# Optimization experiments

Hardware: AMD Instinct MI355X
Metric: run time of the kernel (lower is better)

Reference implementation:

```python
import jax, jax.numpy as jnp
import numpy as np
import math

B, S, HID, NH = 4, 2048, 1024, 16
HD = HID // NH  # head dim = 64


def setup_inputs() -> dict:
    key = jax.random.key(0)
    ks = jax.random.split(key, 8)
    sc = 0.02
    return {
        "x": jax.random.normal(ks[0], (B, S, HID), dtype=jnp.float32),
        "att_mask": jnp.zeros((B, 1, 1, S), dtype=jnp.float32),
        "Wq": jax.random.normal(ks[1], (HID, HID), dtype=jnp.float32) * sc,
        "bq": jax.random.normal(ks[2], (HID,), dtype=jnp.float32) * sc,
        "Wk": jax.random.normal(ks[3], (HID, HID), dtype=jnp.float32) * sc,
        "bk": jax.random.normal(ks[4], (HID,), dtype=jnp.float32) * sc,
        "Wv": jax.random.normal(ks[5], (HID, HID), dtype=jnp.float32) * sc,
        "bv": jax.random.normal(ks[6], (HID,), dtype=jnp.float32) * sc,
    }


def reference(x, att_mask, Wq, bq, Wk, bk, Wv, bv):
    # quant_mode=False path: QuantLinear acts as a plain affine projection
    # (the running min/max stats only calibrate `scale`, which is unused in
    # the float path), and IntSoftmax reduces to a standard softmax.
    q = x @ Wq.T + bq  # [B,S,HID]
    k = x @ Wk.T + bk
    v = x @ Wv.T + bv
    # split heads: [B,S,HID] -> [B,NH,S,HD]
    q = q.reshape(B, S, NH, HD).transpose(0, 2, 1, 3)
    k = k.reshape(B, S, NH, HD).transpose(0, 2, 1, 3)
    v = v.reshape(B, S, NH, HD).transpose(0, 2, 1, 3)
    scores = jnp.einsum("bhqd,bhkd->bhqk", q, k) / math.sqrt(HD) + att_mask
    probs = jax.nn.softmax(scores, axis=-1)  # [B,NH,S,S]
    ctx = jnp.einsum("bhqk,bhkd->bhqd", probs, v)  # [B,NH,S,HD]
    return ctx.transpose(0, 2, 1, 3).reshape(B, S, HID)
```

## Files before the change

### kernel.cpp

```cpp
#include <hip/hip_runtime.h>
#include <hip/hip_bf16.h>
#include <cstdint>
#include <cstddef>

#define BB   4
#define SS   2048
#define HIDD 1024
#define NHH  16
#define HDD  64
#define MM   (BB*SS)
#define L2E  1.4426950408889634f
#define SH4  5.770780163555854f

typedef __bf16    bf16x8 __attribute__((ext_vector_type(8)));
typedef float     f32x4  __attribute__((ext_vector_type(4)));
typedef _Float16  half4  __attribute__((ext_vector_type(4)));
typedef _Float16  half8  __attribute__((ext_vector_type(8)));
typedef _Float16  half2v __attribute__((ext_vector_type(2)));
typedef unsigned  u32x4  __attribute__((ext_vector_type(4)));

__device__ __forceinline__ unsigned short f2b(float f) {
    unsigned u = __builtin_bit_cast(unsigned, f);
    return (unsigned short)((u + 0x7FFFu + ((u >> 16) & 1u)) >> 16);
}

__device__ __forceinline__ half2v pkrtz(float a, float b) {
    return __builtin_bit_cast(half2v, __builtin_amdgcn_cvt_pkrtz(a, b));
}

__device__ __forceinline__ unsigned pkrtz_u(float a, float b) {
    return __builtin_bit_cast(unsigned, __builtin_amdgcn_cvt_pkrtz(a, b));
}

__device__ __forceinline__ void gl_lds16(const void* g, void* l) {
    __builtin_amdgcn_global_load_lds(
        (const __attribute__((address_space(1))) void*)g,
        (__attribute__((address_space(3))) void*)l, 16, 0, 0);
}

#define NX4 (MM * HIDD / 4)
#define NW4 (HIDD * HIDD / 4)
__global__ __launch_bounds__(256) void cvt_all(
    const float* __restrict__ x,  const float* __restrict__ wq,
    const float* __restrict__ wk, const float* __restrict__ wv,
    unsigned short* __restrict__ xb, unsigned short* __restrict__ wb)
{
    int i = blockIdx.x * 256 + threadIdx.x;
    const float* src; unsigned short* dst; int off;
    if (i < NX4) { src = x; dst = xb; off = i; }
    else {
        int j = i - NX4;
        int w = j >> 18;
        off = j & (NW4 - 1);
        src = (w == 0) ? wq : (w == 1) ? wk : wv;
        dst = wb + (size_t)w * HIDD * HIDD;
    }
    float4 v = reinterpret_cast<const float4*>(src)[off];
    ushort4 o;
    o.x = f2b(v.x); o.y = f2b(v.y); o.z = f2b(v.z); o.w = f2b(v.w);
    reinterpret_cast<ushort4*>(dst)[off] = o;
}

__global__ __launch_bounds__(256, 3) void qkv_gemm(
    const unsigned short* __restrict__ xb,
    const unsigned short* __restrict__ wb,
    const float* __restrict__ bq, const float* __restrict__ bk, const float* __restrict__ bv,
    unsigned short* __restrict__ Qb, unsigned short* __restrict__ Kb,
    _Float16* __restrict__ Vtb)
{
    __shared__ unsigned short lA[128 * 64];
    __shared__ unsigned short lB[128 * 64];

    const int tid  = threadIdx.x;
    const int wave = tid >> 6, lane = tid & 63;
    const int lh   = lane & 15, quad = lane >> 4;
    const int l7   = lh & 7;
    const int m0   = blockIdx.x * 128;
    const int opn  = blockIdx.y;
    const int op   = opn >> 3;
    const int n0   = (opn & 7) * 128;
    const unsigned short* W = wb + (size_t)op * HIDD * HIDD;
    const float* bias = (op == 0) ? bq : (op == 1) ? bk : bv;

    f32x4 acc[4][4];
#pragma unroll
    for (int i = 0; i < 4; i++)
#pragma unroll
        for (int j = 0; j < 4; j++) acc[i][j] = f32x4{0.f, 0.f, 0.f, 0.f};

    const int wm = wave & 1, wn = wave >> 1;
    const unsigned short* srcA = (op == 2) ? lA : lB;
    const unsigned short* srcB = (op == 2) ? lB : lA;
    const int offA = (op == 2) ? wm : wn;
    const int offB = (op == 2) ? wn : wm;

    const int srow = tid >> 3;
    const int sg   = tid & 7;

    for (int k0 = 0; k0 < HIDD; k0 += 64) {
#pragma unroll
        for (int rr = 0; rr < 4; rr++) {
            const int row = srow + rr * 32;
            const int gcol = k0 + ((sg ^ (row & 7)) << 3);
            gl_lds16(&xb[(size_t)(m0 + row) * HIDD + gcol], &lA[row * 64 + sg * 8]);
            gl_lds16(&W [(size_t)(n0 + row) * HIDD + gcol], &lB[row * 64 + sg * 8]);
        }
        __syncthreads();

#pragma unroll
        for (int kk = 0; kk < 2; kk++) {
            bf16x8 aF[4], bF[4];
#pragma unroll
            for (int i = 0; i < 4; i++) {
                const int row = offA * 64 + i * 16 + lh;
                aF[i] = *reinterpret_cast<const bf16x8*>(
                    &srcA[row * 64 + (((kk * 4 + quad) ^ l7) << 3)]);
            }
#pragma unroll
            for (int j = 0; j < 4; j++) {
                const int row = offB * 64 + j * 16 + lh;
                bF[j] = *reinterpret_cast<const bf16x8*>(
                    &srcB[row * 64 + (((kk * 4 + quad) ^ l7) << 3)]);
            }
#pragma unroll
            for (int i = 0; i < 4; i++)
#pragma unroll
                for (int j = 0; j < 4; j++)
                    acc[i][j] = __builtin_amdgcn_mfma_f32_16x16x32_bf16(aF[i], bF[j], acc[i][j], 0, 0, 0);
        }
        __syncthreads();
    }

    if (op == 2) {
#pragma unroll
        for (int j = 0; j < 4; j++) {
            const int n = n0 + offB * 64 + j * 16 + lh;
            const float bvv = bias[n];
            const int h = n >> 6, d = n & 63;
#pragma unroll
            for (int i = 0; i < 4; i++) {
                const int mrow = m0 + offA * 64 + i * 16 + quad * 4;
                const int b_ = mrow >> 11, s_ = mrow & 2047;
                half2v h01 = pkrtz(acc[i][j][0] + bvv, acc[i][j][1] + bvv);
                half2v h23 = pkrtz(acc[i][j][2] + bvv, acc[i][j][3] + bvv);
                half4 hv; hv[0] = h01[0]; hv[1] = h01[1]; hv[2] = h23[0]; hv[3] = h23[1];
                size_t a = ((size_t)(b_ * NHH + h) * HDD + d) * SS + s_;
                *reinterpret_cast<half4*>(&Vtb[a]) = hv;
            }
        }
    } else {
        const float qs = (op == 0) ? (0.125f * L2E) : 1.0f;
        unsigned short* dst = (op == 0) ? Qb : Kb;
#pragma unroll
        for (int i = 0; i < 4; i++) {
            const int nb = n0 + offA * 64 + i * 16 + quad * 4;
            const float4 bb = *reinterpret_cast<const float4*>(&bias[nb]);
            const int h = nb >> 6, d = nb & 63;
#pragma unroll
            for (int j = 0; j < 4; j++) {
                const int m = m0 + offB * 64 + j * 16 + lh;
                const int b_ = m >> 11, s_ = m & 2047;
                ushort4 o;
                o.x = f2b((acc[i][j][0] + bb.x) * qs);
                o.y = f2b((acc[i][j][1] + bb.y) * qs);
                o.z = f2b((acc[i][j][2] + bb.z) * qs);
                o.w = f2b((acc[i][j][3] + bb.w) * qs);
                *reinterpret_cast<ushort4*>(
                    &dst[((size_t)(b_ * NHH + h) * SS + s_) * HDD + d]) = o;
            }
        }
    }
}

__global__ __launch_bounds__(256, 4) void attn_kernel(
    const unsigned short* __restrict__ Qb,
    const unsigned short* __restrict__ Kb,
    const _Float16* __restrict__ Vtb,
    const float* __restrict__ mask,
    float* __restrict__ out)
{
    __shared__ unsigned short lK[2][64 * 64];
    __shared__ _Float16      lV[2][64 * 64];
    __shared__ float         lmm[SS];

    const int tid  = threadIdx.x;
    const int wave = tid >> 6, lane = tid & 63;
    const int lh   = lane & 15, quad = lane >> 4;
    const int l7   = lh & 7;
    const int bh = blockIdx.x, qt = blockIdx.y;
    const int b = bh >> 4, h = bh & 15;
    const unsigned short* Qh = Qb  + (size_t)bh * SS * HDD;
    const unsigned short* Kh = Kb  + (size_t)bh * SS * HDD;
    const _Float16*       Vh = Vtb + (size_t)bh * HDD * SS;
    const float* mk = mask + (size_t)b * SS;
    const int q0 = qt * 128;

    bf16x8 qF[2][2];
#pragma unroll
    for (int i = 0; i < 2; i++)
#pragma unroll
        for (int kk = 0; kk < 2; kk++)
            qF[i][kk] = *reinterpret_cast<const bf16x8*>(
                &Qh[(size_t)(q0 + wave * 32 + i * 16 + lh) * HDD + kk * 32 + quad * 8]);

    f32x4 oacc[2][4];
#pragma unroll
    for (int i = 0; i < 2; i++)
#pragma unroll
        for (int dj = 0; dj < 4; dj++) oacc[i][dj] = f32x4{0.f, 0.f, 0.f, 0.f};
    f32x4 osum[2] = {f32x4{0.f, 0.f, 0.f, 0.f}, f32x4{0.f, 0.f, 0.f, 0.f}};

    const u32x4 one_u = {0x3C003C00u, 0x3C003C00u, 0x3C003C00u, 0x3C003C00u};
    const half8 vone  = __builtin_bit_cast(half8, one_u);

    const int srow = tid >> 3;
    const int sg   = tid & 7;

#define STAGE(KT, BUF) do {                                                     \
    const int kb_ = (KT) * 64;                                                  \
    _Pragma("unroll")                                                           \
    for (int rr = 0; rr < 2; rr++) {                                            \
        const int row = srow + rr * 32;                                         \
        const int swk = ((sg ^ ((row & 3) | ((row >> 1) & 4))) << 3);           \
        const int swv = ((sg ^ (row & 7)) << 3);                                \
        gl_lds16(&Kh[(size_t)(kb_ + row) * HDD + swk], &lK[BUF][row * 64 + sg * 8]); \
        gl_lds16(&Vh[(size_t)row * SS + kb_ + swv],    &lV[BUF][row * 64 + sg * 8]); \
    }                                                                           \
} while (0)

    STAGE(0, 0);

#pragma unroll
    for (int j = 0; j < 2; j++) {
        const int idx = tid * 8 + j * 4;
        float4 m = *reinterpret_cast<const float4*>(&mk[idx]);
        float4 r;
        r.x = __builtin_fmaf(m.x, L2E, -SH4);
        r.y = __builtin_fmaf(m.y, L2E, -SH4);
        r.z = __builtin_fmaf(m.z, L2E, -SH4);
        r.w = __builtin_fmaf(m.w, L2E, -SH4);
        *reinterpret_cast<float4*>(&lmm[idx]) = r;
    }
    __syncthreads();

    for (int kt = 0; kt < SS / 64; kt++) {
        if (kt < SS / 64 - 1) STAGE(kt + 1, (kt + 1) & 1);
        const int buf = kt & 1;
        const int kb = kt * 64;

        unsigned pw[2][2][4];
#pragma unroll
        for (int t = 0; t < 2; t++) {
#pragma unroll
            for (int a = 0; a < 2; a++) {
                const int key = t * 32 + ((lh & 12) << 1) + (a << 2) + (lh & 3);
                const int krow = key * 64;
                bf16x8 kf0 = *reinterpret_cast<const bf16x8*>(
                    &lK[buf][krow + ((quad ^ l7) << 3)]);
                bf16x8 kf1 = *reinterpret_cast<const bf16x8*>(
                    &lK[buf][krow + (((4 + quad) ^ l7) << 3)]);
                const f32x4 mm = *reinterpret_cast<const f32x4*>(
                    &lmm[kb + t * 32 + quad * 8 + a * 4]);
#pragma unroll
                for (int i = 0; i < 2; i++) {
                    f32x4 s = __builtin_amdgcn_mfma_f32_16x16x32_bf16(kf0, qF[i][0], mm, 0, 0, 0);
                    s = __builtin_amdgcn_mfma_f32_16x16x32_bf16(kf1, qF[i][1], s, 0, 0, 0);
                    pw[t][i][a * 2 + 0] = pkrtz_u(__builtin_amdgcn_exp2f(s[0]),
                                                  __builtin_amdgcn_exp2f(s[1]));
                    pw[t][i][a * 2 + 1] = pkrtz_u(__builtin_amdgcn_exp2f(s[2]),
                                                  __builtin_amdgcn_exp2f(s[3]));
                }
            }
        }

        __builtin_amdgcn_s_setprio(1);
#pragma unroll
        for (int t = 0; t < 2; t++) {
            half8 vf[4];
#pragma unroll
            for (int dj = 0; dj < 4; dj++)
                vf[dj] = *reinterpret_cast<const half8*>(
                    &lV[buf][(dj * 16 + lh) * 64 + (((t * 4 + quad) ^ l7) << 3)]);
#pragma unroll
            for (int i = 0; i < 2; i++) {
                const u32x4 pu = {pw[t][i][0], pw[t][i][1], pw[t][i][2], pw[t][i][3]};
                const half8 pF = __builtin_bit_cast(half8, pu);
                osum[i] = __builtin_amdgcn_mfma_f32_16x16x32_f16(vone, pF, osum[i], 0, 0, 0);
#pragma unroll
                for (int dj = 0; dj < 4; dj++)
                    oacc[i][dj] = __builtin_amdgcn_mfma_f32_16x16x32_f16(
                        vf[dj], pF, oacc[i][dj], 0, 0, 0);
            }
        }
        __builtin_amdgcn_s_setprio(0);
        if (kt < SS / 64 - 1) __syncthreads();
    }

#pragma unroll
    for (int i = 0; i < 2; i++) {
        const float rls = 1.0f / osum[i][0];
        const int q = q0 + wave * 32 + i * 16 + lh;
#pragma unroll
        for (int dj = 0; dj < 4; dj++) {
            float4 o4;
            o4.x = oacc[i][dj][0] * rls;
            o4.y = oacc[i][dj][1] * rls;
            o4.z = oacc[i][dj][2] * rls;
            o4.w = oacc[i][dj][3] * rls;
            *reinterpret_cast<float4*>(
                &out[((size_t)b * SS + q) * HIDD + h * HDD + dj * 16 + quad * 4]) = o4;
        }
    }
}

extern "C" void kernel_launch(void* const* d_in, const int* in_sizes, int n_in,
                              void* d_out, int out_size, void* d_ws, size_t ws_size,
                              hipStream_t stream) {
    const float* x    = (const float*)d_in[0];
    const float* mask = (const float*)d_in[1];
    const float* Wq   = (const float*)d_in[2];
    const float* bq   = (const float*)d_in[3];
    const float* Wk   = (const float*)d_in[4];
    const float* bk   = (const float*)d_in[5];
    const float* Wv   = (const float*)d_in[6];
    const float* bv   = (const float*)d_in[7];
    float* out = (float*)d_out;
    (void)in_sizes; (void)n_in; (void)out_size; (void)ws_size;

    unsigned short* ws  = (unsigned short*)d_ws;
    unsigned short* xb  = ws;
    unsigned short* wb  = xb + (size_t)MM * HIDD;
    unsigned short* Qb  = wb + (size_t)3 * HIDD * HIDD;
    unsigned short* Kb  = Qb + (size_t)MM * HIDD;
    _Float16*       Vtb = (_Float16*)(Kb + (size_t)MM * HIDD);

    cvt_all<<<(NX4 + 3 * NW4) / 256, 256, 0, stream>>>(x, Wq, Wk, Wv, xb, wb);

    qkv_gemm<<<dim3(MM / 128, 24), 256, 0, stream>>>(xb, wb, bq, bk, bv, Qb, Kb, Vtb);

    attn_kernel<<<dim3(BB * NHH, SS / 128), 256, 0, stream>>>(Qb, Kb, Vtb, mask, out);
}
```

Measured before the change: 236.2 us.

## Software-pipeline attention tile: defer second-half PV MFMA into next iteration

```diff
diff --git a/kernel.cpp b/kernel.cpp
--- a/kernel.cpp
+++ b/kernel.cpp
@@ -228,6 +228,61 @@
     }                                                                           \
 } while (0)
 
+#define A_HALF(T, PF) do {                                                     \
+    _Pragma("unroll")                                                          \
+    for (int a = 0; a < 2; a++) {                                              \
+        const int key = (T) * 32 + ((lh & 12) << 1) + (a << 2) + (lh & 3);     \
+        const int krow = key * 64;                                             \
+        bf16x8 kf0 = *reinterpret_cast<const bf16x8*>(                         \
+            &lK[buf][krow + ((quad ^ l7) << 3)]);                              \
+        bf16x8 kf1 = *reinterpret_cast<const bf16x8*>(                         \
+            &lK[buf][krow + (((4 + quad) ^ l7) << 3)]);                        \
+        const f32x4 mm = *reinterpret_cast<const f32x4*>(                      \
+            &lmm[kb + (T) * 32 + quad * 8 + a * 4]);                           \
+        _Pragma("unroll")                                                      \
+        for (int i = 0; i < 2; i++) {                                          \
+            f32x4 s = __builtin_amdgcn_mfma_f32_16x16x32_bf16(kf0, qF[i][0], mm, 0, 0, 0); \
+            s = __builtin_amdgcn_mfma_f32_16x16x32_bf16(kf1, qF[i][1], s, 0, 0, 0);        \
+            PF[i][a * 2 + 0] = pkrtz_u(__builtin_amdgcn_exp2f(s[0]),           \
+                                       __builtin_amdgcn_exp2f(s[1]));          \
+            PF[i][a * 2 + 1] = pkrtz_u(__builtin_amdgcn_exp2f(s[2]),           \
+                                       __builtin_amdgcn_exp2f(s[3]));          \
+        }                                                                      \
+    }                                                                          \
+} while (0)
+
+#define LOADV(T, VF) do {                                                      \
+    _Pragma("unroll")                                                          \
+    for (int dj = 0; dj < 4; dj++)                                             \
+        VF[dj] = *reinterpret_cast<const half8*>(                              \
+            &lV[buf][(dj * 16 + lh) * 64 + ((((T) * 4 + quad) ^ l7) << 3)]);   \
+} while (0)
+
+#define PV_HALF(PF, VF) do {                                                   \
+    __builtin_amdgcn_s_setprio(1);                                             \
+    _Pragma("unroll")                                                          \
+    for (int i = 0; i < 2; i++) {                                              \
+        const u32x4 pu = {PF[i][0], PF[i][1], PF[i][2], PF[i][3]};             \
+        const half8 pF = __builtin_bit_cast(half8, pu);                        \
+        osum[i] = __builtin_amdgcn_mfma_f32_16x16x32_f16(vone, pF, osum[i], 0, 0, 0); \
+        _Pragma("unroll")                                                      \
+        for (int dj = 0; dj < 4; dj++)                                         \
+            oacc[i][dj] = __builtin_amdgcn_mfma_f32_16x16x32_f16(              \
+                VF[dj], pF, oacc[i][dj], 0, 0, 0);                             \
+    }                                                                          \
+    __builtin_amdgcn_s_setprio(0);                                             \
+} while (0)
+
+    unsigned pfc[2][4];
+    half8    vfc[4];
+#pragma unroll
+    for (int i = 0; i < 2; i++)
+#pragma unroll
+        for (int w = 0; w < 4; w++) pfc[i][w] = 0u;
+#pragma unroll
+    for (int dj = 0; dj < 4; dj++)
+        vfc[dj] = __builtin_bit_cast(half8, u32x4{0u, 0u, 0u, 0u});
+
     STAGE(0, 0);
 
 #pragma unroll
@@ -248,53 +303,20 @@
         const int buf = kt & 1;
         const int kb = kt * 64;
 
-        unsigned pw[2][2][4];
-#pragma unroll
-        for (int t = 0; t < 2; t++) {
-#pragma unroll
-            for (int a = 0; a < 2; a++) {
-                const int key = t * 32 + ((lh & 12) << 1) + (a << 2) + (lh & 3);
-                const int krow = key * 64;
-                bf16x8 kf0 = *reinterpret_cast<const bf16x8*>(
-                    &lK[buf][krow + ((quad ^ l7) << 3)]);
-                bf16x8 kf1 = *reinterpret_cast<const bf16x8*>(
-                    &lK[buf][krow + (((4 + quad) ^ l7) << 3)]);
-                const f32x4 mm = *reinterpret_cast<const f32x4*>(
-                    &lmm[kb + t * 32 + quad * 8 + a * 4]);
-#pragma unroll
-                for (int i = 0; i < 2; i++) {
-                    f32x4 s = __builtin_amdgcn_mfma_f32_16x16x32_bf16(kf0, qF[i][0], mm, 0, 0, 0);
-                    s = __builtin_amdgcn_mfma_f32_16x16x32_bf16(kf1, qF[i][1], s, 0, 0, 0);
-                    pw[t][i][a * 2 + 0] = pkrtz_u(__builtin_amdgcn_exp2f(s[0]),
-                                                  __builtin_amdgcn_exp2f(s[1]));
-                    pw[t][i][a * 2 + 1] = pkrtz_u(__builtin_amdgcn_exp2f(s[2]),
-                                                  __builtin_amdgcn_exp2f(s[3]));
-                }
-            }
-        }
-
-        __builtin_amdgcn_s_setprio(1);
-#pragma unroll
-        for (int t = 0; t < 2; t++) {
-            half8 vf[4];
-#pragma unroll
-            for (int dj = 0; dj < 4; dj++)
-                vf[dj] = *reinterpret_cast<const half8*>(
-                    &lV[buf][(dj * 16 + lh) * 64 + (((t * 4 + quad) ^ l7) << 3)]);
-#pragma unroll
-            for (int i = 0; i < 2; i++) {
-                const u32x4 pu = {pw[t][i][0], pw[t][i][1], pw[t][i][2], pw[t][i][3]};
-                const half8 pF = __builtin_bit_cast(half8, pu);
-                osum[i] = __builtin_amdgcn_mfma_f32_16x16x32_f16(vone, pF, osum[i], 0, 0, 0);
-#pragma unroll
-                for (int dj = 0; dj < 4; dj++)
-                    oacc[i][dj] = __builtin_amdgcn_mfma_f32_16x16x32_f16(
-                        vf[dj], pF, oacc[i][dj], 0, 0, 0);
-            }
-        }
-        __builtin_amdgcn_s_setprio(0);
+        PV_HALF(pfc, vfc);
+
+        unsigned pf0[2][4];
+        A_HALF(0, pf0);
+        half8 vf0[4];
+        LOADV(0, vf0);
+        PV_HALF(pf0, vf0);
+
+        A_HALF(1, pfc);
+        LOADV(1, vfc);
+
         if (kt < SS / 64 - 1) __syncthreads();
     }
+    PV_HALF(pfc, vfc);
 
 #pragma unroll
     for (int i = 0; i < 2; i++) {
@@ -311,6 +333,10 @@
                 &out[((size_t)b * SS + q) * HIDD + h * HDD + dj * 16 + quad * 4]) = o4;
         }
     }
+#undef PV_HALF
+#undef LOADV
+#undef A_HALF
+#undef STAGE
 }
 
 extern "C" void kernel_launch(void* const* d_in, const int* in_sizes, int n_in,
```

New measurement: 235.3 us (median of 3 runs). About the same (-0.4%).

## Double per-wave query rows in attention and read mask directly from global

Applied to the files above, without the earlier changes.

```diff
diff --git a/kernel.cpp b/kernel.cpp
--- a/kernel.cpp
+++ b/kernel.cpp
@@ -172,7 +172,7 @@
     }
 }
 
-__global__ __launch_bounds__(256, 4) void attn_kernel(
+__global__ __launch_bounds__(256, 2) void attn_kernel(
     const unsigned short* __restrict__ Qb,
     const unsigned short* __restrict__ Kb,
     const _Float16* __restrict__ Vtb,
@@ -181,7 +181,6 @@
 {
     __shared__ unsigned short lK[2][64 * 64];
     __shared__ _Float16      lV[2][64 * 64];
-    __shared__ float         lmm[SS];
 
     const int tid  = threadIdx.x;
     const int wave = tid >> 6, lane = tid & 63;
@@ -193,22 +192,24 @@
     const unsigned short* Kh = Kb  + (size_t)bh * SS * HDD;
     const _Float16*       Vh = Vtb + (size_t)bh * HDD * SS;
     const float* mk = mask + (size_t)b * SS;
-    const int q0 = qt * 128;
-
-    bf16x8 qF[2][2];
-#pragma unroll
-    for (int i = 0; i < 2; i++)
+    const int q0 = qt * 256;
+
+    bf16x8 qF[4][2];
+#pragma unroll
+    for (int i = 0; i < 4; i++)
 #pragma unroll
         for (int kk = 0; kk < 2; kk++)
             qF[i][kk] = *reinterpret_cast<const bf16x8*>(
-                &Qh[(size_t)(q0 + wave * 32 + i * 16 + lh) * HDD + kk * 32 + quad * 8]);
-
-    f32x4 oacc[2][4];
-#pragma unroll
-    for (int i = 0; i < 2; i++)
+                &Qh[(size_t)(q0 + wave * 64 + i * 16 + lh) * HDD + kk * 32 + quad * 8]);
+
+    f32x4 oacc[4][4];
+#pragma unroll
+    for (int i = 0; i < 4; i++)
 #pragma unroll
         for (int dj = 0; dj < 4; dj++) oacc[i][dj] = f32x4{0.f, 0.f, 0.f, 0.f};
-    f32x4 osum[2] = {f32x4{0.f, 0.f, 0.f, 0.f}, f32x4{0.f, 0.f, 0.f, 0.f}};
+    f32x4 osum[4];
+#pragma unroll
+    for (int i = 0; i < 4; i++) osum[i] = f32x4{0.f, 0.f, 0.f, 0.f};
 
     const u32x4 one_u = {0x3C003C00u, 0x3C003C00u, 0x3C003C00u, 0x3C003C00u};
     const half8 vone  = __builtin_bit_cast(half8, one_u);
@@ -229,18 +230,6 @@
 } while (0)
 
     STAGE(0, 0);
-
-#pragma unroll
-    for (int j = 0; j < 2; j++) {
-        const int idx = tid * 8 + j * 4;
-        float4 m = *reinterpret_cast<const float4*>(&mk[idx]);
-        float4 r;
-        r.x = __builtin_fmaf(m.x, L2E, -SH4);
-        r.y = __builtin_fmaf(m.y, L2E, -SH4);
-        r.z = __builtin_fmaf(m.z, L2E, -SH4);
-        r.w = __builtin_fmaf(m.w, L2E, -SH4);
-        *reinterpret_cast<float4*>(&lmm[idx]) = r;
-    }
     __syncthreads();
 
     for (int kt = 0; kt < SS / 64; kt++) {
@@ -248,58 +237,67 @@
         const int buf = kt & 1;
         const int kb = kt * 64;
 
-        unsigned pw[2][2][4];
 #pragma unroll
         for (int t = 0; t < 2; t++) {
-#pragma unroll
-            for (int a = 0; a < 2; a++) {
-                const int key = t * 32 + ((lh & 12) << 1) + (a << 2) + (lh & 3);
-                const int krow = key * 64;
-                bf16x8 kf0 = *reinterpret_cast<const bf16x8*>(
-                    &lK[buf][krow + ((quad ^ l7) << 3)]);
-                bf16x8 kf1 = *reinterpret_cast<const bf16x8*>(
-                    &lK[buf][krow + (((4 + quad) ^ l7) << 3)]);
-                const f32x4 mm = *reinterpret_cast<const f32x4*>(
-                    &lmm[kb + t * 32 + quad * 8 + a * 4]);
-#pragma unroll
-                for (int i = 0; i < 2; i++) {
-                    f32x4 s = __builtin_amdgcn_mfma_f32_16x16x32_bf16(kf0, qF[i][0], mm, 0, 0, 0);
-                    s = __builtin_amdgcn_mfma_f32_16x16x32_bf16(kf1, qF[i][1], s, 0, 0, 0);
-                    pw[t][i][a * 2 + 0] = pkrtz_u(__builtin_amdgcn_exp2f(s[0]),
-                                                  __builtin_amdgcn_exp2f(s[1]));
-                    pw[t][i][a * 2 + 1] = pkrtz_u(__builtin_amdgcn_exp2f(s[2]),
-                                                  __builtin_amdgcn_exp2f(s[3]));
-                }
-            }
-        }
-
-        __builtin_amdgcn_s_setprio(1);
-#pragma unroll
-        for (int t = 0; t < 2; t++) {
+            const int keyA = t * 32 + ((lh & 12) << 1) + (lh & 3);
+            const int keyB = keyA + 4;
+            const bf16x8 kfA0 = *reinterpret_cast<const bf16x8*>(
+                &lK[buf][keyA * 64 + ((quad ^ l7) << 3)]);
+            const bf16x8 kfA1 = *reinterpret_cast<const bf16x8*>(
+                &lK[buf][keyA * 64 + (((4 + quad) ^ l7) << 3)]);
+            const bf16x8 kfB0 = *reinterpret_cast<const bf16x8*>(
+                &lK[buf][keyB * 64 + ((quad ^ l7) << 3)]);
+            const bf16x8 kfB1 = *reinterpret_cast<const bf16x8*>(
+                &lK[buf][keyB * 64 + (((4 + quad) ^ l7) << 3)]);
             half8 vf[4];
 #pragma unroll
             for (int dj = 0; dj < 4; dj++)
                 vf[dj] = *reinterpret_cast<const half8*>(
                     &lV[buf][(dj * 16 + lh) * 64 + (((t * 4 + quad) ^ l7) << 3)]);
-#pragma unroll
-            for (int i = 0; i < 2; i++) {
-                const u32x4 pu = {pw[t][i][0], pw[t][i][1], pw[t][i][2], pw[t][i][3]};
+            const float4 mA4 = *reinterpret_cast<const float4*>(&mk[kb + t * 32 + quad * 8]);
+            const float4 mB4 = *reinterpret_cast<const float4*>(&mk[kb + t * 32 + quad * 8 + 4]);
+            f32x4 mmA, mmB;
+            mmA[0] = __builtin_fmaf(mA4.x, L2E, -SH4);
+            mmA[1] = __builtin_fmaf(mA4.y, L2E, -SH4);
+            mmA[2] = __builtin_fmaf(mA4.z, L2E, -SH4);
+            mmA[3] = __builtin_fmaf(mA4.w, L2E, -SH4);
+            mmB[0] = __builtin_fmaf(mB4.x, L2E, -SH4);
+            mmB[1] = __builtin_fmaf(mB4.y, L2E, -SH4);
+            mmB[2] = __builtin_fmaf(mB4.z, L2E, -SH4);
+            mmB[3] = __builtin_fmaf(mB4.w, L2E, -SH4);
+
+#pragma unroll
+            for (int i = 0; i < 4; i++) {
+                f32x4 s0 = __builtin_amdgcn_mfma_f32_16x16x32_bf16(kfA0, qF[i][0], mmA, 0, 0, 0);
+                s0 = __builtin_amdgcn_mfma_f32_16x16x32_bf16(kfA1, qF[i][1], s0, 0, 0, 0);
+                f32x4 s1 = __builtin_amdgcn_mfma_f32_16x16x32_bf16(kfB0, qF[i][0], mmB, 0, 0, 0);
+                s1 = __builtin_amdgcn_mfma_f32_16x16x32_bf16(kfB1, qF[i][1], s1, 0, 0, 0);
+                const unsigned w0 = pkrtz_u(__builtin_amdgcn_exp2f(s0[0]),
+                                            __builtin_amdgcn_exp2f(s0[1]));
+                const unsigned w1 = pkrtz_u(__builtin_amdgcn_exp2f(s0[2]),
+                                            __builtin_amdgcn_exp2f(s0[3]));
+                const unsigned w2 = pkrtz_u(__builtin_amdgcn_exp2f(s1[0]),
+                                            __builtin_amdgcn_exp2f(s1[1]));
+                const unsigned w3 = pkrtz_u(__builtin_amdgcn_exp2f(s1[2]),
+                                            __builtin_amdgcn_exp2f(s1[3]));
+                const u32x4 pu = {w0, w1, w2, w3};
                 const half8 pF = __builtin_bit_cast(half8, pu);
+                __builtin_amdgcn_s_setprio(1);
                 osum[i] = __builtin_amdgcn_mfma_f32_16x16x32_f16(vone, pF, osum[i], 0, 0, 0);
 #pragma unroll
                 for (int dj = 0; dj < 4; dj++)
                     oacc[i][dj] = __builtin_amdgcn_mfma_f32_16x16x32_f16(
                         vf[dj], pF, oacc[i][dj], 0, 0, 0);
-            }
-        }
-        __builtin_amdgcn_s_setprio(0);
+                __builtin_amdgcn_s_setprio(0);
+            }
+        }
         if (kt < SS / 64 - 1) __syncthreads();
     }
 
 #pragma unroll
-    for (int i = 0; i < 2; i++) {
+    for (int i = 0; i < 4; i++) {
         const float rls = 1.0f / osum[i][0];
-        const int q = q0 + wave * 32 + i * 16 + lh;
+        const int q = q0 + wave * 64 + i * 16 + lh;
 #pragma unroll
         for (int dj = 0; dj < 4; dj++) {
             float4 o4;
@@ -311,6 +309,7 @@
                 &out[((size_t)b * SS + q) * HIDD + h * HDD + dj * 16 + quad * 4]) = o4;
         }
     }
+#undef STAGE
 }
 
 extern "C" void kernel_launch(void* const* d_in, const int* in_sizes, int n_in,
@@ -338,5 +337,5 @@
 
     qkv_gemm<<<dim3(MM / 128, 24), 256, 0, stream>>>(xb, wb, bq, bk, bv, Qb, Kb, Vtb);
 
-    attn_kernel<<<dim3(BB * NHH, SS / 128), 256, 0, stream>>>(Qb, Kb, Vtb, mask, out);
-}
+    attn_kernel<<<dim3(BB * NHH, SS / 256), 256, 0, stream>>>(Qb, Kb, Vtb, mask, out);
+}
```

Result: no change. 236.3 us (+0.0%).

## Split attention key tiles across wave pairs and reduce partial outputs via LDS

Applied to the files above, without the earlier changes.

```diff
diff --git a/kernel.cpp b/kernel.cpp
--- a/kernel.cpp
+++ b/kernel.cpp
@@ -172,21 +172,21 @@
     }
 }
 
-__global__ __launch_bounds__(256, 4) void attn_kernel(
+__global__ __launch_bounds__(256, 3) void attn_kernel(
     const unsigned short* __restrict__ Qb,
     const unsigned short* __restrict__ Kb,
     const _Float16* __restrict__ Vtb,
     const float* __restrict__ mask,
     float* __restrict__ out)
 {
-    __shared__ unsigned short lK[2][64 * 64];
-    __shared__ _Float16      lV[2][64 * 64];
-    __shared__ float         lmm[SS];
+    __shared__ float4 smem4[2560];
 
     const int tid  = threadIdx.x;
     const int wave = tid >> 6, lane = tid & 63;
     const int lh   = lane & 15, quad = lane >> 4;
     const int l7   = lh & 7;
+    const int qw   = wave & 1;
+    const int kw   = wave >> 1;
     const int bh = blockIdx.x, qt = blockIdx.y;
     const int b = bh >> 4, h = bh & 15;
     const unsigned short* Qh = Qb  + (size_t)bh * SS * HDD;
@@ -195,26 +195,28 @@
     const float* mk = mask + (size_t)b * SS;
     const int q0 = qt * 128;
 
-    bf16x8 qF[2][2];
-#pragma unroll
-    for (int i = 0; i < 2; i++)
+    float* lmm = (float*)(smem4 + 2048);
+
+    bf16x8 qF[4][2];
+#pragma unroll
+    for (int i = 0; i < 4; i++)
 #pragma unroll
         for (int kk = 0; kk < 2; kk++)
             qF[i][kk] = *reinterpret_cast<const bf16x8*>(
-                &Qh[(size_t)(q0 + wave * 32 + i * 16 + lh) * HDD + kk * 32 + quad * 8]);
-
-    f32x4 oacc[2][4];
-#pragma unroll
-    for (int i = 0; i < 2; i++)
+                &Qh[(size_t)(q0 + qw * 64 + i * 16 + lh) * HDD + kk * 32 + quad * 8]);
+
+    f32x4 oacc[4][4];
+#pragma unroll
+    for (int i = 0; i < 4; i++)
 #pragma unroll
         for (int dj = 0; dj < 4; dj++) oacc[i][dj] = f32x4{0.f, 0.f, 0.f, 0.f};
-    f32x4 osum[2] = {f32x4{0.f, 0.f, 0.f, 0.f}, f32x4{0.f, 0.f, 0.f, 0.f}};
-
-    const u32x4 one_u = {0x3C003C00u, 0x3C003C00u, 0x3C003C00u, 0x3C003C00u};
-    const half8 vone  = __builtin_bit_cast(half8, one_u);
+    float ls[4] = {0.f, 0.f, 0.f, 0.f};
 
     const int srow = tid >> 3;
     const int sg   = tid & 7;
+
+#define LKP(BUF) ((unsigned short*)smem4 + (BUF) * 4096)
+#define LVP(BUF) ((_Float16*)(smem4 + 1024) + (BUF) * 4096)
 
 #define STAGE(KT, BUF) do {                                                     \
     const int kb_ = (KT) * 64;                                                  \
@@ -223,8 +225,8 @@
         const int row = srow + rr * 32;                                         \
         const int swk = ((sg ^ ((row & 3) | ((row >> 1) & 4))) << 3);           \
         const int swv = ((sg ^ (row & 7)) << 3);                                \
-        gl_lds16(&Kh[(size_t)(kb_ + row) * HDD + swk], &lK[BUF][row * 64 + sg * 8]); \
-        gl_lds16(&Vh[(size_t)row * SS + kb_ + swv],    &lV[BUF][row * 64 + sg * 8]); \
+        gl_lds16(&Kh[(size_t)(kb_ + row) * HDD + swk], LKP(BUF) + row * 64 + sg * 8); \
+        gl_lds16(&Vh[(size_t)row * SS + kb_ + swv],    LVP(BUF) + row * 64 + sg * 8); \
     }                                                                           \
 } while (0)
 
@@ -247,70 +249,99 @@
         if (kt < SS / 64 - 1) STAGE(kt + 1, (kt + 1) & 1);
         const int buf = kt & 1;
         const int kb = kt * 64;
-
-        unsigned pw[2][2][4];
-#pragma unroll
-        for (int t = 0; t < 2; t++) {
-#pragma unroll
-            for (int a = 0; a < 2; a++) {
-                const int key = t * 32 + ((lh & 12) << 1) + (a << 2) + (lh & 3);
-                const int krow = key * 64;
-                bf16x8 kf0 = *reinterpret_cast<const bf16x8*>(
-                    &lK[buf][krow + ((quad ^ l7) << 3)]);
-                bf16x8 kf1 = *reinterpret_cast<const bf16x8*>(
-                    &lK[buf][krow + (((4 + quad) ^ l7) << 3)]);
-                const f32x4 mm = *reinterpret_cast<const f32x4*>(
-                    &lmm[kb + t * 32 + quad * 8 + a * 4]);
-#pragma unroll
-                for (int i = 0; i < 2; i++) {
-                    f32x4 s = __builtin_amdgcn_mfma_f32_16x16x32_bf16(kf0, qF[i][0], mm, 0, 0, 0);
-                    s = __builtin_amdgcn_mfma_f32_16x16x32_bf16(kf1, qF[i][1], s, 0, 0, 0);
-                    pw[t][i][a * 2 + 0] = pkrtz_u(__builtin_amdgcn_exp2f(s[0]),
-                                                  __builtin_amdgcn_exp2f(s[1]));
-                    pw[t][i][a * 2 + 1] = pkrtz_u(__builtin_amdgcn_exp2f(s[2]),
-                                                  __builtin_amdgcn_exp2f(s[3]));
-                }
-            }
-        }
+        const unsigned short* lK_ = LKP(buf);
+        const _Float16*       lV_ = LVP(buf);
+
+        unsigned pf[4][4];
+#pragma unroll
+        for (int a = 0; a < 2; a++) {
+            const int key = kw * 32 + ((lh & 12) << 1) + (a << 2) + (lh & 3);
+            const int krow = key * 64;
+            bf16x8 kf0 = *reinterpret_cast<const bf16x8*>(
+                &lK_[krow + ((quad ^ l7) << 3)]);
+            bf16x8 kf1 = *reinterpret_cast<const bf16x8*>(
+                &lK_[krow + (((4 + quad) ^ l7) << 3)]);
+            const f32x4 mm = *reinterpret_cast<const f32x4*>(
+                &lmm[kb + kw * 32 + quad * 8 + a * 4]);
+#pragma unroll
+            for (int i = 0; i < 4; i++) {
+                f32x4 s = __builtin_amdgcn_mfma_f32_16x16x32_bf16(kf0, qF[i][0], mm, 0, 0, 0);
+                s = __builtin_amdgcn_mfma_f32_16x16x32_bf16(kf1, qF[i][1], s, 0, 0, 0);
+                float e0 = __builtin_amdgcn_exp2f(s[0]);
+                float e1 = __builtin_amdgcn_exp2f(s[1]);
+                float e2 = __builtin_amdgcn_exp2f(s[2]);
+                float e3 = __builtin_amdgcn_exp2f(s[3]);
+                ls[i] += (e0 + e1) + (e2 + e3);
+                pf[i][a * 2 + 0] = pkrtz_u(e0, e1);
+                pf[i][a * 2 + 1] = pkrtz_u(e2, e3);
+            }
+        }
+
+        half8 vf[4];
+#pragma unroll
+        for (int dj = 0; dj < 4; dj++)
+            vf[dj] = *reinterpret_cast<const half8*>(
+                &lV_[(dj * 16 + lh) * 64 + (((kw * 4 + quad) ^ l7) << 3)]);
 
         __builtin_amdgcn_s_setprio(1);
 #pragma unroll
-        for (int t = 0; t < 2; t++) {
-            half8 vf[4];
+        for (int i = 0; i < 4; i++) {
+            const u32x4 pu = {pf[i][0], pf[i][1], pf[i][2], pf[i][3]};
+            const half8 pF = __builtin_bit_cast(half8, pu);
 #pragma unroll
             for (int dj = 0; dj < 4; dj++)
-                vf[dj] = *reinterpret_cast<const half8*>(
-                    &lV[buf][(dj * 16 + lh) * 64 + (((t * 4 + quad) ^ l7) << 3)]);
-#pragma unroll
-            for (int i = 0; i < 2; i++) {
-                const u32x4 pu = {pw[t][i][0], pw[t][i][1], pw[t][i][2], pw[t][i][3]};
-                const half8 pF = __builtin_bit_cast(half8, pu);
-                osum[i] = __builtin_amdgcn_mfma_f32_16x16x32_f16(vone, pF, osum[i], 0, 0, 0);
-#pragma unroll
-                for (int dj = 0; dj < 4; dj++)
-                    oacc[i][dj] = __builtin_amdgcn_mfma_f32_16x16x32_f16(
-                        vf[dj], pF, oacc[i][dj], 0, 0, 0);
-            }
+                oacc[i][dj] = __builtin_amdgcn_mfma_f32_16x16x32_f16(
+                    vf[dj], pF, oacc[i][dj], 0, 0, 0);
         }
         __builtin_amdgcn_s_setprio(0);
+
         if (kt < SS / 64 - 1) __syncthreads();
     }
 
 #pragma unroll
-    for (int i = 0; i < 2; i++) {
-        const float rls = 1.0f / osum[i][0];
-        const int q = q0 + wave * 32 + i * 16 + lh;
-#pragma unroll
-        for (int dj = 0; dj < 4; dj++) {
-            float4 o4;
-            o4.x = oacc[i][dj][0] * rls;
-            o4.y = oacc[i][dj][1] * rls;
-            o4.z = oacc[i][dj][2] * rls;
-            o4.w = oacc[i][dj][3] * rls;
-            *reinterpret_cast<float4*>(
-                &out[((size_t)b * SS + q) * HIDD + h * HDD + dj * 16 + quad * 4]) = o4;
-        }
-    }
+    for (int i = 0; i < 4; i++) {
+        ls[i] += __shfl_xor(ls[i], 16);
+        ls[i] += __shfl_xor(ls[i], 32);
+    }
+
+    __syncthreads();
+    if (kw == 1) {
+#pragma unroll
+        for (int i = 0; i < 4; i++)
+#pragma unroll
+            for (int dj = 0; dj < 4; dj++)
+                smem4[(i * 4 + dj) * 128 + qw * 64 + lane] =
+                    __builtin_bit_cast(float4, oacc[i][dj]);
+        float4 lsp; lsp.x = ls[0]; lsp.y = ls[1]; lsp.z = ls[2]; lsp.w = ls[3];
+        smem4[16 * 128 + qw * 64 + lane] = lsp;
+    }
+    __syncthreads();
+    if (kw == 0) {
+        const float4 lsp = smem4[16 * 128 + qw * 64 + lane];
+        float rls[4];
+        rls[0] = 1.0f / (ls[0] + lsp.x);
+        rls[1] = 1.0f / (ls[1] + lsp.y);
+        rls[2] = 1.0f / (ls[2] + lsp.z);
+        rls[3] = 1.0f / (ls[3] + lsp.w);
+#pragma unroll
+        for (int i = 0; i < 4; i++) {
+            const int q = q0 + qw * 64 + i * 16 + lh;
+#pragma unroll
+            for (int dj = 0; dj < 4; dj++) {
+                const float4 p = smem4[(i * 4 + dj) * 128 + qw * 64 + lane];
+                float4 o4;
+                o4.x = (oacc[i][dj][0] + p.x) * rls[i];
+                o4.y = (oacc[i][dj][1] + p.y) * rls[i];
+                o4.z = (oacc[i][dj][2] + p.z) * rls[i];
+                o4.w = (oacc[i][dj][3] + p.w) * rls[i];
+                *reinterpret_cast<float4*>(
+                    &out[((size_t)b * SS + q) * HIDD + h * HDD + dj * 16 + quad * 4]) = o4;
+            }
+        }
+    }
+#undef STAGE
+#undef LKP
+#undef LVP
 }
 
 extern "C" void kernel_launch(void* const* d_in, const int* in_sizes, int n_in,
```

Result: no change. 240.2 us (+1.7%).
